# Kernel tuning notes

Hardware: AMD Instinct MI355X
Metric: run time of the kernel (lower is better)

Reference implementation:

```python
import jax, jax.numpy as jnp
import numpy as np

TEMPERATURE = 0.5
EPS = 1e-8  # torch.nn.CosineSimilarity eps


def _l2norm(x):
    # torch cosine sim divides by max(||x||, eps) per vector
    n = jnp.sqrt(jnp.sum(x * x, axis=-1, keepdims=True))
    return x / jnp.maximum(n, EPS)


def setup_inputs() -> dict:
    key = jax.random.key(0)
    ka, kb = jax.random.split(key)
    batch_a = jax.random.normal(ka, (4096, 512), dtype=jnp.float32)
    batch_b = jax.random.normal(kb, (4096, 512), dtype=jnp.float32)
    return {"batch_a": batch_a, "batch_b": batch_b}


def reference(batch_a, batch_b):
    a = _l2norm(batch_a)  # [N, D]
    b = _l2norm(batch_b)
    inv_t = 1.0 / TEMPERATURE
    # cosine similarity via normalize + GEMM (same math as broadcast mul+reduce)
    sim11 = (a @ a.T) * inv_t  # [N, N]
    sim22 = (b @ b.T) * inv_t
    sim12 = (a @ b.T) * inv_t
    n = sim12.shape[-1]
    eye = jnp.eye(n, dtype=bool)
    neg_inf = jnp.float32(-jnp.inf)
    sim11 = jnp.where(eye, neg_inf, sim11)
    sim22 = jnp.where(eye, neg_inf, sim22)
    # logits: [[sim12, sim11], [sim22, sim12^T]] -> [2N, 2N]
    logits = jnp.concatenate(
        [jnp.concatenate([sim12, sim11], axis=-1),
         jnp.concatenate([sim22, sim12.T], axis=-1)],
        axis=-2,
    )
    targets = jnp.arange(2 * n)
    logp = jax.nn.log_softmax(logits, axis=-1)  # stable single pass
    loss = -jnp.mean(logp[jnp.arange(2 * n), targets])
    return loss
```

## Files before the change

kernel.cpp:

```cpp
#include <hip/hip_runtime.h>

#define NR 4096
#define DD 512
#define TWO_N 8192
#define MT2 32
#define NT2 528
#define CH2 66

using bf16x8 = __attribute__((ext_vector_type(8))) short;
using f32x4  = __attribute__((ext_vector_type(4))) float;

__device__ __forceinline__ unsigned short f2bf(float f) {
    union { float f; unsigned u; } v; v.f = f;
    unsigned r = v.u + 0x7fff + ((v.u >> 16) & 1);
    return (unsigned short)(r >> 16);
}

__global__ __launch_bounds__(256) void ntx_nrm_kernel(const float* __restrict__ A,
                                                      const float* __restrict__ B,
                                                      unsigned short* __restrict__ X,
                                                      float* __restrict__ d12,
                                                      float* __restrict__ S) {
    const int row = blockIdx.x;
    const int t = threadIdx.x;
    const int lane = t & 63, wid = t >> 6;

    if (t < 2) S[row * 2 + t] = 0.f;

    const float2 av = *(const float2*)(A + row * DD + 2 * t);
    const float2 bv = *(const float2*)(B + row * DD + 2 * t);
    float sa = av.x * av.x + av.y * av.y;
    float sb = bv.x * bv.x + bv.y * bv.y;
#pragma unroll
    for (int o = 32; o; o >>= 1) { sa += __shfl_down(sa, o); sb += __shfl_down(sb, o); }

    __shared__ float red[12];
    if (lane == 0) { red[wid] = sa; red[4 + wid] = sb; }
    __syncthreads();
    const float ta = red[0] + red[1] + red[2] + red[3];
    const float tb = red[4] + red[5] + red[6] + red[7];
    const float ra = 1.f / fmaxf(sqrtf(ta), 1e-8f);
    const float rb = 1.f / fmaxf(sqrtf(tb), 1e-8f);
    const float nax = av.x * ra, nay = av.y * ra;
    const float nbx = bv.x * rb, nby = bv.y * rb;

    *(unsigned*)(X + row * DD + 2 * t) =
        (unsigned)f2bf(nax) | ((unsigned)f2bf(nay) << 16);
    *(unsigned*)(X + (NR + row) * DD + 2 * t) =
        (unsigned)f2bf(nbx) | ((unsigned)f2bf(nby) << 16);

    float dt = nax * nbx + nay * nby;
#pragma unroll
    for (int o = 32; o; o >>= 1) dt += __shfl_down(dt, o);
    if (lane == 0) red[8 + wid] = dt;
    __syncthreads();
    if (t == 0) d12[row] = red[8] + red[9] + red[10] + red[11];
}

__global__ __launch_bounds__(512, 2) void ntx_gemm_lse_kernel(const unsigned short* __restrict__ X,
                                                              float* __restrict__ S) {
    const int bid = blockIdx.x;
    const int sid = (bid & 7) * CH2 + (bid >> 3);
    int u, v;
    if (sid < 448) {
        const int s = sid >> 4, loc = sid & 15;
        int U = 0;
        while (7 * (U + 1) - (U + 1) * U / 2 <= s) ++U;
        const int V = U + 1 + (s - (7 * U - U * (U - 1) / 2));
        u = U * 4 + (loc >> 2);
        v = V * 4 + (loc & 3);
    } else {
        const int s2 = sid - 448;
        const int U = s2 / 10, loc = s2 % 10;
        int lu = 0;
        while ((lu + 1) * 4 - (lu + 1) * lu / 2 <= loc) ++lu;
        const int lv = lu + (loc - (lu * 4 - lu * (lu - 1) / 2));
        u = U * 4 + lu;
        v = U * 4 + lv;
    }
    const bool fixedTile = (u == v);
    const int rowTile = u * 256, colTile = (v ^ 16) * 256;

    __shared__ unsigned short As[4][256 * 32];
    __shared__ unsigned short Bs[4][256 * 32];

    const int t = threadIdx.x;
    const int lane = t & 63, wid = t >> 6;
    const int waveM = wid >> 2, waveN = wid & 3;
    const int lr = lane & 15, grp = lane >> 4;
    const int swr = (lr >> 1) & 3;
    const int kslot = (grp ^ swr) * 8;

    f32x4 acc[8][4] = {};

    const int srow = lane >> 2;
    const int scol = ((lane & 3) ^ ((lane >> 3) & 3)) * 8;

    auto STAGE_A = [&](int sel, int kt) {
#pragma unroll
        for (int q = 0; q < 2; ++q) {
            const int ci = wid * 2 + q;
            const int r  = ci * 16 + srow;
            __builtin_amdgcn_global_load_lds(
                (const __attribute__((address_space(1))) unsigned*)(X + (size_t)(rowTile + r) * DD + kt + scol),
                (__attribute__((address_space(3))) unsigned*)&As[sel][ci * 512 + lane * 8], 16, 0, 0);
        }
    };
    auto STAGE_B = [&](int sel, int kt) {
#pragma unroll
        for (int q = 0; q < 2; ++q) {
            const int ci = wid * 2 + q;
            const int r  = ci * 16 + srow;
            __builtin_amdgcn_global_load_lds(
                (const __attribute__((address_space(1))) unsigned*)(X + (size_t)((colTile + r) ^ NR) * DD + kt + scol),
                (__attribute__((address_space(3))) unsigned*)&Bs[sel][ci * 512 + lane * 8], 16, 0, 0);
        }
    };

    auto PHASE = [&](int sel, int mbase, bf16x8* bfr) {
        bf16x8 af[4];
#pragma unroll
        for (int mm = 0; mm < 4; ++mm)
            af[mm] = *(const bf16x8*)&As[sel][(waveM * 128 + (mbase + mm) * 16 + lr) * 32 + kslot];
        __builtin_amdgcn_s_setprio(1);
#pragma unroll
        for (int mm = 0; mm < 4; ++mm)
#pragma unroll
            for (int n = 0; n < 4; ++n)
                acc[mbase + mm][n] = __builtin_amdgcn_mfma_f32_16x16x32_bf16(af[mm], bfr[n], acc[mbase + mm][n], 0, 0, 0);
        __builtin_amdgcn_s_setprio(0);
    };

    STAGE_A(0, 0);   STAGE_B(0, 0);
    STAGE_A(1, 32);  STAGE_B(1, 32);
    STAGE_A(2, 64);  STAGE_B(2, 64);

#pragma unroll
    for (int tt = 0; tt < 16; ++tt) {
        const int sel = tt & 3;
        asm volatile("s_waitcnt lgkmcnt(0)" ::: "memory");
        if (tt <= 13)      asm volatile("s_waitcnt vmcnt(8)" ::: "memory");
        else if (tt == 14) asm volatile("s_waitcnt vmcnt(4)" ::: "memory");
        else               asm volatile("s_waitcnt vmcnt(0)" ::: "memory");
        __builtin_amdgcn_s_barrier();
        bf16x8 bfr[4];
#pragma unroll
        for (int n = 0; n < 4; ++n)
            bfr[n] = *(const bf16x8*)&Bs[sel][(waveN * 64 + n * 16 + lr) * 32 + kslot];
        if (tt < 13) STAGE_A((tt + 3) & 3, (tt + 3) * 32);
        PHASE(sel, 0, bfr);
        if (tt < 13) STAGE_B((tt + 3) & 3, (tt + 3) * 32);
        PHASE(sel, 4, bfr);
    }

#pragma unroll
    for (int m = 0; m < 8; ++m)
#pragma unroll
        for (int n = 0; n < 4; ++n)
#pragma unroll
            for (int reg = 0; reg < 4; ++reg) {
                const int R = rowTile + waveM * 128 + m * 16 + grp * 4 + reg;
                const int C = colTile + waveN * 64 + n * 16 + lr;
                const bool masked = fixedTile && (C == (R ^ NR));
                acc[m][n][reg] = masked ? 0.f : __expf(acc[m][n][reg] * 2.0f);
            }

#pragma unroll
    for (int m = 0; m < 8; ++m)
#pragma unroll
        for (int reg = 0; reg < 4; ++reg) {
            float rs = acc[m][0][reg] + acc[m][1][reg] + acc[m][2][reg] + acc[m][3][reg];
            rs += __shfl_xor(rs, 1);
            rs += __shfl_xor(rs, 2);
            rs += __shfl_xor(rs, 4);
            rs += __shfl_xor(rs, 8);
            if (lr == 0) {
                const int R = rowTile + waveM * 128 + m * 16 + grp * 4 + reg;
                atomicAdd(&S[R], rs);
            }
        }

    if (!fixedTile) {
#pragma unroll
        for (int n = 0; n < 4; ++n) {
            float cs = 0.f;
#pragma unroll
            for (int m = 0; m < 8; ++m)
#pragma unroll
                for (int reg = 0; reg < 4; ++reg)
                    cs += acc[m][n][reg];
            cs += __shfl_xor(cs, 16);
            cs += __shfl_xor(cs, 32);
            if (grp == 0) {
                const int C = colTile + waveN * 64 + n * 16 + lr;
                atomicAdd(&S[C ^ NR], cs);
            }
        }
    }
}

__global__ __launch_bounds__(256) void ntx_loss_kernel(const float* __restrict__ S,
                                                       const float* __restrict__ d12,
                                                       float* __restrict__ out) {
    const int t = threadIdx.x;
    float a = 0.f;
    for (int r = t; r < TWO_N; r += 256)
        a += __logf(S[r]) - 2.0f * d12[r & (NR - 1)];
    const int lane = t & 63, wid = t >> 6;
#pragma unroll
    for (int o = 32; o; o >>= 1) a += __shfl_down(a, o);
    __shared__ float red[4];
    if (lane == 0) red[wid] = a;
    __syncthreads();
    if (t == 0) out[0] = (red[0] + red[1] + red[2] + red[3]) * (1.f / (float)TWO_N);
}

extern "C" void kernel_launch(void* const* d_in, const int* in_sizes, int n_in,
                              void* d_out, int out_size, void* d_ws, size_t ws_size,
                              hipStream_t stream) {
    const float* A = (const float*)d_in[0];
    const float* B = (const float*)d_in[1];

    unsigned short* X = (unsigned short*)d_ws;
    float* S   = (float*)((char*)d_ws + (size_t)TWO_N * DD * 2);
    float* d12 = (float*)((char*)S + (size_t)TWO_N * 4);

    ntx_nrm_kernel<<<NR, 256, 0, stream>>>(A, B, X, d12, S);

    ntx_gemm_lse_kernel<<<NT2, 512, 0, stream>>>(X, S);

    ntx_loss_kernel<<<1, 256, 0, stream>>>(S, d12, (float*)d_out);
}
```

Baseline: 90.15 us.

## Restructure GEMM to BK=64 double buffer with quadrant-interleaved MFMA schedule

The GEMM+LSE kernel moves from a 4-stage BK=32 ring to a 2-stage BK=64 double buffer with a new XOR swizzle. Each K-step is split into four MFMA quadrants, with LDS fragment loads and the next tile's global-to-LDS copies interleaved between them. The launch bound drops to one block per CU because LDS use doubles. Separately, the final loss reduction is spread across 32 blocks that combine into the output with atomics, and the output is zeroed with a memset first. This trades occupancy and extra barriers for longer K-steps and finer load/compute overlap.

New measurement: 86.87 us. 3.6% less time.

```diff
diff --git a/kernel.cpp b/kernel.cpp
--- a/kernel.cpp
+++ b/kernel.cpp
@@ -57,7 +57,7 @@
     if (t == 0) d12[row] = red[8] + red[9] + red[10] + red[11];
 }
 
-__global__ __launch_bounds__(512, 2) void ntx_gemm_lse_kernel(const unsigned short* __restrict__ X,
+__global__ __launch_bounds__(512, 1) void ntx_gemm_lse_kernel(const unsigned short* __restrict__ X,
                                                               float* __restrict__ S) {
     const int bid = blockIdx.x;
     const int sid = (bid & 7) * CH2 + (bid >> 3);
@@ -81,76 +81,94 @@
     const bool fixedTile = (u == v);
     const int rowTile = u * 256, colTile = (v ^ 16) * 256;
 
-    __shared__ unsigned short As[4][256 * 32];
-    __shared__ unsigned short Bs[4][256 * 32];
+    __shared__ unsigned short As[2][256 * 64];
+    __shared__ unsigned short Bs[2][256 * 64];
 
     const int t = threadIdx.x;
     const int lane = t & 63, wid = t >> 6;
     const int waveM = wid >> 2, waveN = wid & 3;
     const int lr = lane & 15, grp = lane >> 4;
-    const int swr = (lr >> 1) & 3;
-    const int kslot = (grp ^ swr) * 8;
+    const int r3 = lr & 7;
 
     f32x4 acc[8][4] = {};
-
-    const int srow = lane >> 2;
-    const int scol = ((lane & 3) ^ ((lane >> 3) & 3)) * 8;
-
-    auto STAGE_A = [&](int sel, int kt) {
-#pragma unroll
-        for (int q = 0; q < 2; ++q) {
-            const int ci = wid * 2 + q;
-            const int r  = ci * 16 + srow;
-            __builtin_amdgcn_global_load_lds(
-                (const __attribute__((address_space(1))) unsigned*)(X + (size_t)(rowTile + r) * DD + kt + scol),
-                (__attribute__((address_space(3))) unsigned*)&As[sel][ci * 512 + lane * 8], 16, 0, 0);
-        }
-    };
-    auto STAGE_B = [&](int sel, int kt) {
-#pragma unroll
-        for (int q = 0; q < 2; ++q) {
-            const int ci = wid * 2 + q;
-            const int r  = ci * 16 + srow;
-            __builtin_amdgcn_global_load_lds(
-                (const __attribute__((address_space(1))) unsigned*)(X + (size_t)((colTile + r) ^ NR) * DD + kt + scol),
-                (__attribute__((address_space(3))) unsigned*)&Bs[sel][ci * 512 + lane * 8], 16, 0, 0);
-        }
-    };
-
-    auto PHASE = [&](int sel, int mbase, bf16x8* bfr) {
-        bf16x8 af[4];
+    bf16x8 af[4][2];
+    bf16x8 bf[4][2];
+
+    const int srow = lane >> 3;
+    const int scol = ((lane & 7) ^ srow) * 8;
+
+    auto STAGE1 = [&](int sel, int kt, int q) {
+        const int ci = wid * 4 + q;
+        const int r  = ci * 8 + srow;
+        const int lo = ci * 512 + lane * 8;
+        __builtin_amdgcn_global_load_lds(
+            (const __attribute__((address_space(1))) unsigned*)(X + (size_t)(rowTile + r) * DD + kt + scol),
+            (__attribute__((address_space(3))) unsigned*)&As[sel][lo], 16, 0, 0);
+        __builtin_amdgcn_global_load_lds(
+            (const __attribute__((address_space(1))) unsigned*)(X + (size_t)((colTile + r) ^ NR) * DD + kt + scol),
+            (__attribute__((address_space(3))) unsigned*)&Bs[sel][lo], 16, 0, 0);
+    };
+
+    auto LDA = [&](int sel, int mh) {
 #pragma unroll
         for (int mm = 0; mm < 4; ++mm)
-            af[mm] = *(const bf16x8*)&As[sel][(waveM * 128 + (mbase + mm) * 16 + lr) * 32 + kslot];
+#pragma unroll
+            for (int kk = 0; kk < 2; ++kk)
+                af[mm][kk] = *(const bf16x8*)&As[sel][(waveM * 128 + (mh * 4 + mm) * 16 + lr) * 64 +
+                                                      (((kk * 4 + grp) ^ r3) * 8)];
+    };
+    auto LDB = [&](int sel, int nh) {
+#pragma unroll
+        for (int nn = 0; nn < 2; ++nn)
+#pragma unroll
+            for (int kk = 0; kk < 2; ++kk)
+                bf[nh * 2 + nn][kk] = *(const bf16x8*)&Bs[sel][(waveN * 64 + (nh * 2 + nn) * 16 + lr) * 64 +
+                                                               (((kk * 4 + grp) ^ r3) * 8)];
+    };
+    auto QUAD = [&](int mh, int nh) {
         __builtin_amdgcn_s_setprio(1);
 #pragma unroll
         for (int mm = 0; mm < 4; ++mm)
 #pragma unroll
-            for (int n = 0; n < 4; ++n)
-                acc[mbase + mm][n] = __builtin_amdgcn_mfma_f32_16x16x32_bf16(af[mm], bfr[n], acc[mbase + mm][n], 0, 0, 0);
+            for (int nn = 0; nn < 2; ++nn)
+#pragma unroll
+                for (int kk = 0; kk < 2; ++kk)
+                    acc[mh * 4 + mm][nh * 2 + nn] = __builtin_amdgcn_mfma_f32_16x16x32_bf16(
+                        af[mm][kk], bf[nh * 2 + nn][kk], acc[mh * 4 + mm][nh * 2 + nn], 0, 0, 0);
         __builtin_amdgcn_s_setprio(0);
     };
 
-    STAGE_A(0, 0);   STAGE_B(0, 0);
-    STAGE_A(1, 32);  STAGE_B(1, 32);
-    STAGE_A(2, 64);  STAGE_B(2, 64);
-
-#pragma unroll
-    for (int tt = 0; tt < 16; ++tt) {
-        const int sel = tt & 3;
+    STAGE1(0, 0, 0); STAGE1(0, 0, 1); STAGE1(0, 0, 2); STAGE1(0, 0, 3);
+    asm volatile("s_waitcnt vmcnt(0)" ::: "memory");
+    __builtin_amdgcn_s_barrier();
+
+    for (int tt = 0; tt < 8; ++tt) {
+        const int sel = tt & 1;
+        const int kn = (tt + 1) * 64;
+        LDA(sel, 0); LDB(sel, 0);
+        if (tt < 7) { STAGE1(sel ^ 1, kn, 0); STAGE1(sel ^ 1, kn, 1); }
+        __builtin_amdgcn_s_barrier();
         asm volatile("s_waitcnt lgkmcnt(0)" ::: "memory");
-        if (tt <= 13)      asm volatile("s_waitcnt vmcnt(8)" ::: "memory");
-        else if (tt == 14) asm volatile("s_waitcnt vmcnt(4)" ::: "memory");
-        else               asm volatile("s_waitcnt vmcnt(0)" ::: "memory");
-        __builtin_amdgcn_s_barrier();
-        bf16x8 bfr[4];
-#pragma unroll
-        for (int n = 0; n < 4; ++n)
-            bfr[n] = *(const bf16x8*)&Bs[sel][(waveN * 64 + n * 16 + lr) * 32 + kslot];
-        if (tt < 13) STAGE_A((tt + 3) & 3, (tt + 3) * 32);
-        PHASE(sel, 0, bfr);
-        if (tt < 13) STAGE_B((tt + 3) & 3, (tt + 3) * 32);
-        PHASE(sel, 4, bfr);
+        __builtin_amdgcn_sched_barrier(0);
+        QUAD(0, 0);
+        __builtin_amdgcn_s_barrier();
+        LDB(sel, 1);
+        if (tt < 7) STAGE1(sel ^ 1, kn, 2);
+        __builtin_amdgcn_s_barrier();
+        asm volatile("s_waitcnt lgkmcnt(0)" ::: "memory");
+        __builtin_amdgcn_sched_barrier(0);
+        QUAD(0, 1);
+        __builtin_amdgcn_s_barrier();
+        LDA(sel, 1);
+        if (tt < 7) STAGE1(sel ^ 1, kn, 3);
+        __builtin_amdgcn_s_barrier();
+        asm volatile("s_waitcnt lgkmcnt(0)" ::: "memory");
+        __builtin_amdgcn_sched_barrier(0);
+        QUAD(1, 1);
+        __builtin_amdgcn_s_barrier();
+        QUAD(1, 0);
+        if (tt < 7) asm volatile("s_waitcnt vmcnt(0)" ::: "memory");
+        __builtin_amdgcn_s_barrier();
     }
 
 #pragma unroll
@@ -203,16 +221,15 @@
                                                        const float* __restrict__ d12,
                                                        float* __restrict__ out) {
     const int t = threadIdx.x;
-    float a = 0.f;
-    for (int r = t; r < TWO_N; r += 256)
-        a += __logf(S[r]) - 2.0f * d12[r & (NR - 1)];
+    const int r = blockIdx.x * 256 + t;
+    float a = __logf(S[r]) - 2.0f * d12[r & (NR - 1)];
     const int lane = t & 63, wid = t >> 6;
 #pragma unroll
     for (int o = 32; o; o >>= 1) a += __shfl_down(a, o);
     __shared__ float red[4];
     if (lane == 0) red[wid] = a;
     __syncthreads();
-    if (t == 0) out[0] = (red[0] + red[1] + red[2] + red[3]) * (1.f / (float)TWO_N);
+    if (t == 0) atomicAdd(out, (red[0] + red[1] + red[2] + red[3]) * (1.f / (float)TWO_N));
 }
 
 extern "C" void kernel_launch(void* const* d_in, const int* in_sizes, int n_in,
@@ -225,9 +242,11 @@
     float* S   = (float*)((char*)d_ws + (size_t)TWO_N * DD * 2);
     float* d12 = (float*)((char*)S + (size_t)TWO_N * 4);
 
+    hipMemsetAsync(d_out, 0, sizeof(float), stream);
+
     ntx_nrm_kernel<<<NR, 256, 0, stream>>>(A, B, X, d12, S);
 
     ntx_gemm_lse_kernel<<<NT2, 512, 0, stream>>>(X, S);
 
-    ntx_loss_kernel<<<1, 256, 0, stream>>>(S, d12, (float*)d_out);
-}
+    ntx_loss_kernel<<<TWO_N / 256, 256, 0, stream>>>(S, d12, (float*)d_out);
+}
```
